# Kernel tuning notes

Measured on AMD Instinct MI355X. Metric: run time of the kernel, lower is better.

The kernel has to match this reference:

```python
import jax, jax.numpy as jnp
import numpy as np

T, K, E, H, I = 1024, 2, 8, 2048, 768


def setup_inputs() -> dict:
    key = jax.random.key(0)
    k1, k2, k3, k4, k5 = jax.random.split(key, 5)
    hidden_states = jax.random.normal(k1, (T, H), dtype=jnp.float32)
    top_k_index = jax.random.randint(k2, (T, K), 0, E)
    logits = jax.random.normal(k3, (T, K), dtype=jnp.float32)
    top_k_weights = jax.nn.softmax(logits, axis=-1)  # realistic routing weights
    # Linear-style weights: gate_up [E, 2I, H], down [E, H, I]; scaled like trained params
    gate_up_proj = jax.random.normal(k4, (E, 2 * I, H), dtype=jnp.float32) * 0.02
    down_proj = jax.random.normal(k5, (E, H, I), dtype=jnp.float32) * 0.02
    return {
        "hidden_states": hidden_states,
        "top_k_index": top_k_index,
        "top_k_weights": top_k_weights,
        "gate_up_proj": gate_up_proj,
        "down_proj": down_proj,
    }


def reference(hidden_states, top_k_index, top_k_weights, gate_up_proj, down_proj):
    """Dense-dispatch MoE forward: same math as the per-expert 4-bit loop.

    For every token t and routed expert e (with routing weight w):
      gate, up = split(x_t @ Wgu_e^T); y_t += w * (silu(gate)*up) @ Wd_e^T
    Expressed densely over experts; non-routed (token, expert) pairs get a
    combine weight of 0, so they contribute nothing.
    """
    num_experts = gate_up_proj.shape[0]
    # combine[t, e] = sum_k w[t,k] * [top_k_index[t,k] == e]
    combine = jnp.sum(
        jax.nn.one_hot(top_k_index, num_experts, dtype=hidden_states.dtype)
        * top_k_weights[..., None],
        axis=1,
    )  # [T, E]
    # gate_up: [T, E, 2I]
    gu = jnp.einsum("th,eoh->teo", hidden_states, gate_up_proj)
    gate, up = jnp.split(gu, 2, axis=-1)
    h = jax.nn.silu(gate) * up  # [T, E, I]
    # fold combine weight in before the down projection (scalar per (t,e))
    h = h * combine[:, :, None]
    out = jnp.einsum("tei,ehi->th", h, down_proj)  # [T, H]
    return out.astype(hidden_states.dtype)
```

## Files before the change

kernel.cpp:

```cpp
#include <hip/hip_runtime.h>
#include <hip/hip_bf16.h>

#define T_TOK 1024
#define TOPK  2
#define NEXP  8
#define HDIM  2048
#define IDIM  768
#define MROW  384

typedef __attribute__((ext_vector_type(4))) float f32x4;
typedef __attribute__((ext_vector_type(8))) short bf16x8;
typedef __attribute__((ext_vector_type(8))) unsigned short u16x8;
typedef __attribute__((ext_vector_type(8))) __bf16 bfv8;

__device__ __forceinline__ bf16x8 cvt8(f32x4 v0, f32x4 v1) {
  bfv8 r;
#pragma unroll
  for (int j = 0; j < 4; ++j) { r[j] = (__bf16)v0[j]; r[4 + j] = (__bf16)v1[j]; }
  return __builtin_bit_cast(bf16x8, r);
}

__device__ __forceinline__ void gload_lds16(const void* g, void* l) {
  __builtin_amdgcn_global_load_lds(
      (const __attribute__((address_space(1))) unsigned int*)((unsigned long long)g),
      (__attribute__((address_space(3))) unsigned int*)(unsigned int)(unsigned long long)(l),
      16, 0, 0);
}


__global__ void k_gather(const int* __restrict__ idx, const float* __restrict__ wts,
                         int* __restrict__ cnt, int* __restrict__ tok,
                         float* __restrict__ wl, int* __restrict__ inv) {
  int g = blockIdx.x * 256 + threadIdx.x;
  int e = idx[g];
  float w = wts[g];
  int pos = atomicAdd(&cnt[e], 1);
  if (pos < 2048) { tok[e * 2048 + pos] = g; wl[e * 2048 + pos] = w; }
  inv[g] = (pos < MROW) ? (e * MROW + pos) : -1;
}

__global__ __launch_bounds__(256) void k_compact(const float* __restrict__ x,
                                                 const int* __restrict__ inv,
                                                 unsigned short* __restrict__ xe) {
  int pid = blockIdx.x;
  int iv = inv[pid];
  if (iv < 0) return;
  const float* src = x + (size_t)(pid >> 1) * HDIM;
  unsigned short* dst = xe + (size_t)iv * HDIM;
  int i = threadIdx.x * 8;
  f32x4 a = *(const f32x4*)(src + i);
  f32x4 b = *(const f32x4*)(src + i + 4);
  *(u16x8*)(dst + i) = __builtin_bit_cast(u16x8, cvt8(a, b));
}

__global__ __launch_bounds__(256, 3) void k_gate_up(
    const unsigned short* __restrict__ xe, const float* __restrict__ Wgu,
    const int* __restrict__ cnt, const float* __restrict__ wl,
    unsigned short* __restrict__ hb)
{
  const int b = blockIdx.x;
  const int e = b & 7;
  const int r = b >> 3;
  const int mt = r % 6;
  const int nb = r / 6;
  const int m0 = mt * 64;
  int cc = cnt[e]; if (cc > MROW) cc = MROW;
  if (m0 >= cc) return;
  const int col0 = nb * 32;

  __shared__ unsigned short sA[3 * 4096];
  __shared__ unsigned short sB[3 * 4096];
  __shared__ float sW[64];

  const int tid = threadIdx.x;
  const int lane = tid & 63, wid = tid >> 6;

  if (tid < 64) sW[tid] = (m0 + tid < cc) ? wl[e * 2048 + m0 + tid] : 0.f;

  const unsigned short* xeE = xe + ((size_t)e * MROW + m0) * HDIM;
  const unsigned short* aSrc[2];
  unsigned int aDstOff[2];
#pragma unroll
  for (int i = 0; i < 2; ++i) {
    int row = wid * 16 + i * 8 + (lane >> 3);
    int csrc = (lane & 7) ^ (row & 7);
    aSrc[i] = xeE + (size_t)row * HDIM + csrc * 8;
    aDstOff[i] = (unsigned)(wid * 16 + i * 8) * 64;
  }

  const int brow = tid >> 2, cq = (tid & 3);
  const int ocol = (brow < 32) ? (col0 + brow) : (IDIM + col0 + (brow - 32));
  const float* bSrc = Wgu + ((size_t)e * 2 * IDIM + ocol) * HDIM + cq * 16;
  unsigned int bDst[2];
#pragma unroll
  for (int c2 = 0; c2 < 2; ++c2)
    bDst[c2] = (unsigned)(brow * 64 + (((cq * 2 + c2) ^ (brow & 7)) * 8));

  const int fl = lane & 15, q = lane >> 4;
  const int wm = (wid >> 1) * 32, wn = (wid & 1) * 16;

  f32x4 accg[2], accu[2];
#pragma unroll
  for (int mf = 0; mf < 2; ++mf) {
    accg[mf] = f32x4{0.f, 0.f, 0.f, 0.f};
    accu[mf] = f32x4{0.f, 0.f, 0.f, 0.f};
  }

  f32x4 blA[4], blB[4];
  const int NS = HDIM / 64;

  auto COMPUTE = [&](int bo) {
    const unsigned short* A = sA + bo;
    const unsigned short* B = sB + bo;
#pragma unroll
    for (int s = 0; s < 2; ++s) {
      bf16x8 a[2], g2, u2;
#pragma unroll
      for (int mf = 0; mf < 2; ++mf) {
        int rr = wm + mf * 16 + fl;
        a[mf] = *(const bf16x8*)(A + rr * 64 + (((s * 4 + q) ^ (rr & 7)) * 8));
      }
      {
        int rg = wn + fl;
        g2 = *(const bf16x8*)(B + rg * 64 + (((s * 4 + q) ^ (rg & 7)) * 8));
        int ru = 32 + wn + fl;
        u2 = *(const bf16x8*)(B + ru * 64 + (((s * 4 + q) ^ (ru & 7)) * 8));
      }
#pragma unroll
      for (int mf = 0; mf < 2; ++mf) {
        accg[mf] = __builtin_amdgcn_mfma_f32_16x16x32_bf16(a[mf], g2, accg[mf], 0, 0, 0);
        accu[mf] = __builtin_amdgcn_mfma_f32_16x16x32_bf16(a[mf], u2, accu[mf], 0, 0, 0);
      }
    }
  };

  auto ITER = [&](int ks, f32x4 (&blR)[4], f32x4 (&blW)[4],
                  int oC, int oN, int oNN) {
    const bool nL = (ks + 2) < NS;
    const bool nW = (ks + 1) < NS;
    if (nL) {
#pragma unroll
      for (int i = 0; i < 2; ++i)
        gload_lds16(aSrc[i] + (ks + 2) * 64, &sA[oNN + aDstOff[i]]);
#pragma unroll
      for (int j = 0; j < 4; ++j)
        blW[j] = *(const f32x4*)(bSrc + (ks + 2) * 64 + j * 4);
    }
    if (nW) {
#pragma unroll
      for (int c2 = 0; c2 < 2; ++c2)
        *(bf16x8*)&sB[oN + bDst[c2]] = cvt8(blR[c2 * 2], blR[c2 * 2 + 1]);
    }
    COMPUTE(oC);
    if (nW) {
      if (nL) { asm volatile("s_waitcnt vmcnt(6) lgkmcnt(0)" ::: "memory"); }
      else    { asm volatile("s_waitcnt vmcnt(0) lgkmcnt(0)" ::: "memory"); }
      __builtin_amdgcn_sched_barrier(0);
      __builtin_amdgcn_s_barrier();
      __builtin_amdgcn_sched_barrier(0);
    }
  };

#pragma unroll
  for (int i = 0; i < 2; ++i) gload_lds16(aSrc[i], &sA[aDstOff[i]]);
#pragma unroll
  for (int j = 0; j < 4; ++j) blA[j] = *(const f32x4*)(bSrc + j * 4);
#pragma unroll
  for (int i = 0; i < 2; ++i) gload_lds16(aSrc[i] + 64, &sA[4096 + aDstOff[i]]);
#pragma unroll
  for (int j = 0; j < 4; ++j) blB[j] = *(const f32x4*)(bSrc + 64 + j * 4);
#pragma unroll
  for (int c2 = 0; c2 < 2; ++c2)
    *(bf16x8*)&sB[bDst[c2]] = cvt8(blA[c2 * 2], blA[c2 * 2 + 1]);
  asm volatile("s_waitcnt vmcnt(6) lgkmcnt(0)" ::: "memory");
  __builtin_amdgcn_sched_barrier(0);
  __builtin_amdgcn_s_barrier();
  __builtin_amdgcn_sched_barrier(0);

  int oC = 0, oN = 4096, oNN = 8192;
  for (int ks = 0; ks < NS; ks += 2) {
    ITER(ks, blB, blA, oC, oN, oNN);
    int t = oC; oC = oN; oN = oNN; oNN = t;
    ITER(ks + 1, blA, blB, oC, oN, oNN);
    t = oC; oC = oN; oN = oNN; oNN = t;
  }

  unsigned short* hbE = hb + (size_t)e * MROW * IDIM;
  const int q4 = q * 4;
#pragma unroll
  for (int mf = 0; mf < 2; ++mf)
#pragma unroll
    for (int v = 0; v < 4; ++v) {
      int rowl = wm + mf * 16 + q4 + v;
      if (m0 + rowl < cc) {
        float g = accg[mf][v], u = accu[mf][v];
        float s = g / (1.f + __expf(-g));
        float h = s * u * sW[rowl];
        hbE[(size_t)(m0 + rowl) * IDIM + col0 + wn + fl] =
            __builtin_bit_cast(unsigned short, (__bf16)h);
      }
    }
}

__global__ __launch_bounds__(256, 3) void k_down(
    const unsigned short* __restrict__ hb, const float* __restrict__ Wd,
    const int* __restrict__ cnt, const int* __restrict__ tok,
    float* __restrict__ out)
{
  const int b = blockIdx.x;
  const int e = b & 7;
  const int r = b >> 3;
  const int mt = r % 6;
  const int nb = r / 6;
  const int m0 = mt * 64;
  int cc = cnt[e]; if (cc > MROW) cc = MROW;
  if (m0 >= cc) return;
  const int col0 = nb * 64;

  __shared__ unsigned short sA[3 * 4096];
  __shared__ unsigned short sB[3 * 4096];
  __shared__ int sTok[64];

  const int tid = threadIdx.x;
  const int lane = tid & 63, wid = tid >> 6;
  if (tid < 64) sTok[tid] = (m0 + tid < cc) ? (tok[e * 2048 + m0 + tid] >> 1) : 0;

  const unsigned short* hbE = hb + ((size_t)e * MROW + m0) * IDIM;
  const unsigned short* aSrc[2];
  unsigned int aDstOff[2];
#pragma unroll
  for (int i = 0; i < 2; ++i) {
    int row = wid * 16 + i * 8 + (lane >> 3);
    int csrc = (lane & 7) ^ (row & 7);
    aSrc[i] = hbE + (size_t)row * IDIM + csrc * 8;
    aDstOff[i] = (unsigned)(wid * 16 + i * 8) * 64;
  }

  const int brow = tid >> 2, cq = (tid & 3);
  const float* bSrc = Wd + ((size_t)e * HDIM + col0 + brow) * IDIM + cq * 16;
  unsigned int bDst[2];
#pragma unroll
  for (int c2 = 0; c2 < 2; ++c2)
    bDst[c2] = (unsigned)(brow * 64 + (((cq * 2 + c2) ^ (brow & 7)) * 8));

  const int fl = lane & 15, q = lane >> 4;
  const int wm = (wid >> 1) * 32, wn = (wid & 1) * 32;

  f32x4 acc[2][2];
#pragma unroll
  for (int mf = 0; mf < 2; ++mf)
#pragma unroll
    for (int nf = 0; nf < 2; ++nf) acc[mf][nf] = f32x4{0.f, 0.f, 0.f, 0.f};

  f32x4 blA[4], blB[4];
  const int NS = IDIM / 64;

  auto COMPUTE = [&](int bo) {
    const unsigned short* A = sA + bo;
    const unsigned short* B = sB + bo;
#pragma unroll
    for (int s = 0; s < 2; ++s) {
      bf16x8 a[2], bb[2];
#pragma unroll
      for (int mf = 0; mf < 2; ++mf) {
        int rr = wm + mf * 16 + fl;
        a[mf] = *(const bf16x8*)(A + rr * 64 + (((s * 4 + q) ^ (rr & 7)) * 8));
      }
#pragma unroll
      for (int nf = 0; nf < 2; ++nf) {
        int rn = wn + nf * 16 + fl;
        bb[nf] = *(const bf16x8*)(B + rn * 64 + (((s * 4 + q) ^ (rn & 7)) * 8));
      }
#pragma unroll
      for (int mf = 0; mf < 2; ++mf)
#pragma unroll
        for (int nf = 0; nf < 2; ++nf)
          acc[mf][nf] = __builtin_amdgcn_mfma_f32_16x16x32_bf16(a[mf], bb[nf], acc[mf][nf], 0, 0, 0);
    }
  };

  auto ITER = [&](int ks, f32x4 (&blR)[4], f32x4 (&blW)[4],
                  int oC, int oN, int oNN) {
    const bool nL = (ks + 2) < NS;
    const bool nW = (ks + 1) < NS;
    if (nL) {
#pragma unroll
      for (int i = 0; i < 2; ++i)
        gload_lds16(aSrc[i] + (ks + 2) * 64, &sA[oNN + aDstOff[i]]);
#pragma unroll
      for (int j = 0; j < 4; ++j)
        blW[j] = *(const f32x4*)(bSrc + (ks + 2) * 64 + j * 4);
    }
    if (nW) {
#pragma unroll
      for (int c2 = 0; c2 < 2; ++c2)
        *(bf16x8*)&sB[oN + bDst[c2]] = cvt8(blR[c2 * 2], blR[c2 * 2 + 1]);
    }
    COMPUTE(oC);
    if (nW) {
      if (nL) { asm volatile("s_waitcnt vmcnt(6) lgkmcnt(0)" ::: "memory"); }
      else    { asm volatile("s_waitcnt vmcnt(0) lgkmcnt(0)" ::: "memory"); }
      __builtin_amdgcn_sched_barrier(0);
      __builtin_amdgcn_s_barrier();
      __builtin_amdgcn_sched_barrier(0);
    }
  };

#pragma unroll
  for (int i = 0; i < 2; ++i) gload_lds16(aSrc[i], &sA[aDstOff[i]]);
#pragma unroll
  for (int j = 0; j < 4; ++j) blA[j] = *(const f32x4*)(bSrc + j * 4);
#pragma unroll
  for (int i = 0; i < 2; ++i) gload_lds16(aSrc[i] + 64, &sA[4096 + aDstOff[i]]);
#pragma unroll
  for (int j = 0; j < 4; ++j) blB[j] = *(const f32x4*)(bSrc + 64 + j * 4);
#pragma unroll
  for (int c2 = 0; c2 < 2; ++c2)
    *(bf16x8*)&sB[bDst[c2]] = cvt8(blA[c2 * 2], blA[c2 * 2 + 1]);
  asm volatile("s_waitcnt vmcnt(6) lgkmcnt(0)" ::: "memory");
  __builtin_amdgcn_sched_barrier(0);
  __builtin_amdgcn_s_barrier();
  __builtin_amdgcn_sched_barrier(0);

  int oC = 0, oN = 4096, oNN = 8192;
  for (int ks = 0; ks < NS; ks += 2) {
    ITER(ks, blB, blA, oC, oN, oNN);
    int t = oC; oC = oN; oN = oNN; oNN = t;
    ITER(ks + 1, blA, blB, oC, oN, oNN);
    t = oC; oC = oN; oN = oNN; oNN = t;
  }

  const int q4 = q * 4;
#pragma unroll
  for (int mf = 0; mf < 2; ++mf)
#pragma unroll
    for (int nf = 0; nf < 2; ++nf)
#pragma unroll
      for (int v = 0; v < 4; ++v) {
        int rowl = wm + mf * 16 + q4 + v;
        if (m0 + rowl < cc) {
          int t = sTok[rowl];
          atomicAdd(out + (size_t)t * HDIM + col0 + wn + nf * 16 + fl, acc[mf][nf][v]);
        }
      }
}

extern "C" void kernel_launch(void* const* d_in, const int* in_sizes, int n_in,
                              void* d_out, int out_size, void* d_ws, size_t ws_size,
                              hipStream_t stream) {
  const float* x   = (const float*)d_in[0];
  const int*   idx = (const int*)d_in[1];
  const float* wts = (const float*)d_in[2];
  const float* Wgu = (const float*)d_in[3];
  const float* Wd  = (const float*)d_in[4];
  float* out = (float*)d_out;

  char* ws = (char*)d_ws;
  int*            cnt = (int*)(ws + 0);
  int*            tok = (int*)(ws + 64);
  float*          wl  = (float*)(ws + 65600);
  int*            inv = (int*)(ws + 131136);
  unsigned short* xe  = (unsigned short*)(ws + 139328);
  unsigned short* hb  = (unsigned short*)(ws + 12722240);

  hipMemsetAsync(cnt, 0, NEXP * sizeof(int), stream);
  hipMemsetAsync(out, 0, (size_t)T_TOK * HDIM * sizeof(float), stream);
  k_gather<<<dim3((T_TOK * TOPK) / 256), 256, 0, stream>>>(idx, wts, cnt, tok, wl, inv);
  k_compact<<<dim3(T_TOK * TOPK), 256, 0, stream>>>(x, inv, xe);
  k_gate_up<<<dim3(NEXP * 6 * 24), 256, 0, stream>>>(xe, Wgu, cnt, wl, hb);
  k_down<<<dim3(NEXP * 6 * 32), 256, 0, stream>>>(hb, Wd, cnt, tok, out);
}
```

Baseline: 119.6 us.

## Enlarge gate_up M tile to 128 rows and simplify to double buffering

The gate_up kernel now covers 128 token rows per block instead of 64, so each fp32 weight tile loaded and converted is reused across twice as many rows, and the grid is halved. The triple-buffered pipeline with hand-placed waitcnt and barriers is replaced by a plain double-buffered loop synchronized with __syncthreads, and the occupancy hint in launch bounds is dropped. This cuts the redundant weight traffic, which dominates since weights are read in fp32, but gives up some load/compute overlap and leaves fewer blocks to fill the GPU.

New measurement: 108.7 us. 1.1x faster.

```diff
diff --git a/kernel.cpp b/kernel.cpp
--- a/kernel.cpp
+++ b/kernel.cpp
@@ -50,10 +50,10 @@
   int i = threadIdx.x * 8;
   f32x4 a = *(const f32x4*)(src + i);
   f32x4 b = *(const f32x4*)(src + i + 4);
-  *(u16x8*)(dst + i) = __builtin_bit_cast(u16x8, cvt8(a, b));
-}
-
-__global__ __launch_bounds__(256, 3) void k_gate_up(
+  *(bf16x8*)(dst + i) = cvt8(a, b);
+}
+
+__global__ __launch_bounds__(256) void k_gate_up(
     const unsigned short* __restrict__ xe, const float* __restrict__ Wgu,
     const int* __restrict__ cnt, const float* __restrict__ wl,
     unsigned short* __restrict__ hb)
@@ -61,31 +61,31 @@
   const int b = blockIdx.x;
   const int e = b & 7;
   const int r = b >> 3;
-  const int mt = r % 6;
-  const int nb = r / 6;
-  const int m0 = mt * 64;
+  const int mt = r % 3;
+  const int nb = r / 3;
+  const int m0 = mt * 128;
   int cc = cnt[e]; if (cc > MROW) cc = MROW;
   if (m0 >= cc) return;
   const int col0 = nb * 32;
 
-  __shared__ unsigned short sA[3 * 4096];
-  __shared__ unsigned short sB[3 * 4096];
-  __shared__ float sW[64];
+  __shared__ unsigned short sA[2][128 * 64];
+  __shared__ unsigned short sB[2][64 * 64];
+  __shared__ float sW[128];
 
   const int tid = threadIdx.x;
   const int lane = tid & 63, wid = tid >> 6;
 
-  if (tid < 64) sW[tid] = (m0 + tid < cc) ? wl[e * 2048 + m0 + tid] : 0.f;
+  if (tid < 128) sW[tid] = (m0 + tid < cc) ? wl[e * 2048 + m0 + tid] : 0.f;
 
   const unsigned short* xeE = xe + ((size_t)e * MROW + m0) * HDIM;
-  const unsigned short* aSrc[2];
-  unsigned int aDstOff[2];
-#pragma unroll
-  for (int i = 0; i < 2; ++i) {
-    int row = wid * 16 + i * 8 + (lane >> 3);
+  const unsigned short* aSrc[4];
+  unsigned int aDstOff[4];
+#pragma unroll
+  for (int i = 0; i < 4; ++i) {
+    int row = wid * 32 + i * 8 + (lane >> 3);
     int csrc = (lane & 7) ^ (row & 7);
     aSrc[i] = xeE + (size_t)row * HDIM + csrc * 8;
-    aDstOff[i] = (unsigned)(wid * 16 + i * 8) * 64;
+    aDstOff[i] = (unsigned)(wid * 32 + i * 8) * 64;
   }
 
   const int brow = tid >> 2, cq = (tid & 3);
@@ -97,28 +97,40 @@
     bDst[c2] = (unsigned)(brow * 64 + (((cq * 2 + c2) ^ (brow & 7)) * 8));
 
   const int fl = lane & 15, q = lane >> 4;
-  const int wm = (wid >> 1) * 32, wn = (wid & 1) * 16;
-
-  f32x4 accg[2], accu[2];
-#pragma unroll
-  for (int mf = 0; mf < 2; ++mf) {
-    accg[mf] = f32x4{0.f, 0.f, 0.f, 0.f};
-    accu[mf] = f32x4{0.f, 0.f, 0.f, 0.f};
-  }
-
-  f32x4 blA[4], blB[4];
-  const int NS = HDIM / 64;
-
-  auto COMPUTE = [&](int bo) {
-    const unsigned short* A = sA + bo;
-    const unsigned short* B = sB + bo;
+  const int wm = (wid >> 1) * 64, wn = (wid & 1) * 16;
+
+  f32x4 accg[4], accu[4];
+#pragma unroll
+  for (int rf = 0; rf < 4; ++rf) {
+    accg[rf] = f32x4{0.f, 0.f, 0.f, 0.f};
+    accu[rf] = f32x4{0.f, 0.f, 0.f, 0.f};
+  }
+
+  f32x4 bl[4];
+
+  auto STAGE_ISSUE = [&](int buf, int kt) {
+#pragma unroll
+    for (int i = 0; i < 4; ++i)
+      gload_lds16(aSrc[i] + kt, &sA[buf][aDstOff[i]]);
+#pragma unroll
+    for (int j = 0; j < 4; ++j)
+      bl[j] = *(const f32x4*)(bSrc + kt + j * 4);
+  };
+  auto STAGE_WRITE = [&](int buf) {
+#pragma unroll
+    for (int c2 = 0; c2 < 2; ++c2)
+      *(bf16x8*)&sB[buf][bDst[c2]] = cvt8(bl[c2 * 2], bl[c2 * 2 + 1]);
+  };
+  auto COMPUTE = [&](int buf) {
+    const unsigned short* A = sA[buf];
+    const unsigned short* B = sB[buf];
 #pragma unroll
     for (int s = 0; s < 2; ++s) {
-      bf16x8 a[2], g2, u2;
-#pragma unroll
-      for (int mf = 0; mf < 2; ++mf) {
-        int rr = wm + mf * 16 + fl;
-        a[mf] = *(const bf16x8*)(A + rr * 64 + (((s * 4 + q) ^ (rr & 7)) * 8));
+      bf16x8 a[4], g2, u2;
+#pragma unroll
+      for (int rf = 0; rf < 4; ++rf) {
+        int rr = wm + rf * 16 + fl;
+        a[rf] = *(const bf16x8*)(A + rr * 64 + (((s * 4 + q) ^ (rr & 7)) * 8));
       }
       {
         int rg = wn + fl;
@@ -127,73 +139,36 @@
         u2 = *(const bf16x8*)(B + ru * 64 + (((s * 4 + q) ^ (ru & 7)) * 8));
       }
 #pragma unroll
-      for (int mf = 0; mf < 2; ++mf) {
-        accg[mf] = __builtin_amdgcn_mfma_f32_16x16x32_bf16(a[mf], g2, accg[mf], 0, 0, 0);
-        accu[mf] = __builtin_amdgcn_mfma_f32_16x16x32_bf16(a[mf], u2, accu[mf], 0, 0, 0);
-      }
-    }
-  };
-
-  auto ITER = [&](int ks, f32x4 (&blR)[4], f32x4 (&blW)[4],
-                  int oC, int oN, int oNN) {
-    const bool nL = (ks + 2) < NS;
-    const bool nW = (ks + 1) < NS;
-    if (nL) {
-#pragma unroll
-      for (int i = 0; i < 2; ++i)
-        gload_lds16(aSrc[i] + (ks + 2) * 64, &sA[oNN + aDstOff[i]]);
-#pragma unroll
-      for (int j = 0; j < 4; ++j)
-        blW[j] = *(const f32x4*)(bSrc + (ks + 2) * 64 + j * 4);
-    }
-    if (nW) {
-#pragma unroll
-      for (int c2 = 0; c2 < 2; ++c2)
-        *(bf16x8*)&sB[oN + bDst[c2]] = cvt8(blR[c2 * 2], blR[c2 * 2 + 1]);
-    }
-    COMPUTE(oC);
-    if (nW) {
-      if (nL) { asm volatile("s_waitcnt vmcnt(6) lgkmcnt(0)" ::: "memory"); }
-      else    { asm volatile("s_waitcnt vmcnt(0) lgkmcnt(0)" ::: "memory"); }
-      __builtin_amdgcn_sched_barrier(0);
-      __builtin_amdgcn_s_barrier();
-      __builtin_amdgcn_sched_barrier(0);
-    }
-  };
-
-#pragma unroll
-  for (int i = 0; i < 2; ++i) gload_lds16(aSrc[i], &sA[aDstOff[i]]);
-#pragma unroll
-  for (int j = 0; j < 4; ++j) blA[j] = *(const f32x4*)(bSrc + j * 4);
-#pragma unroll
-  for (int i = 0; i < 2; ++i) gload_lds16(aSrc[i] + 64, &sA[4096 + aDstOff[i]]);
-#pragma unroll
-  for (int j = 0; j < 4; ++j) blB[j] = *(const f32x4*)(bSrc + 64 + j * 4);
-#pragma unroll
-  for (int c2 = 0; c2 < 2; ++c2)
-    *(bf16x8*)&sB[bDst[c2]] = cvt8(blA[c2 * 2], blA[c2 * 2 + 1]);
-  asm volatile("s_waitcnt vmcnt(6) lgkmcnt(0)" ::: "memory");
-  __builtin_amdgcn_sched_barrier(0);
-  __builtin_amdgcn_s_barrier();
-  __builtin_amdgcn_sched_barrier(0);
-
-  int oC = 0, oN = 4096, oNN = 8192;
-  for (int ks = 0; ks < NS; ks += 2) {
-    ITER(ks, blB, blA, oC, oN, oNN);
-    int t = oC; oC = oN; oN = oNN; oNN = t;
-    ITER(ks + 1, blA, blB, oC, oN, oNN);
-    t = oC; oC = oN; oN = oNN; oNN = t;
+      for (int rf = 0; rf < 4; ++rf) {
+        accg[rf] = __builtin_amdgcn_mfma_f32_16x16x32_bf16(a[rf], g2, accg[rf], 0, 0, 0);
+        accu[rf] = __builtin_amdgcn_mfma_f32_16x16x32_bf16(a[rf], u2, accu[rf], 0, 0, 0);
+      }
+    }
+  };
+
+  STAGE_ISSUE(0, 0);
+  STAGE_WRITE(0);
+  __syncthreads();
+  int buf = 0;
+  for (int kt = 0; kt < HDIM; kt += 64) {
+    const int nxt = kt + 64;
+    const bool more = nxt < HDIM;
+    if (more) STAGE_ISSUE(buf ^ 1, nxt);
+    COMPUTE(buf);
+    if (more) STAGE_WRITE(buf ^ 1);
+    __syncthreads();
+    buf ^= 1;
   }
 
   unsigned short* hbE = hb + (size_t)e * MROW * IDIM;
   const int q4 = q * 4;
 #pragma unroll
-  for (int mf = 0; mf < 2; ++mf)
+  for (int rf = 0; rf < 4; ++rf)
 #pragma unroll
     for (int v = 0; v < 4; ++v) {
-      int rowl = wm + mf * 16 + q4 + v;
+      int rowl = wm + rf * 16 + q4 + v;
       if (m0 + rowl < cc) {
-        float g = accg[mf][v], u = accu[mf][v];
+        float g = accg[rf][v], u = accu[rf][v];
         float s = g / (1.f + __expf(-g));
         float h = s * u * sW[rowl];
         hbE[(size_t)(m0 + rowl) * IDIM + col0 + wn + fl] =
@@ -367,6 +342,6 @@
   hipMemsetAsync(out, 0, (size_t)T_TOK * HDIM * sizeof(float), stream);
   k_gather<<<dim3((T_TOK * TOPK) / 256), 256, 0, stream>>>(idx, wts, cnt, tok, wl, inv);
   k_compact<<<dim3(T_TOK * TOPK), 256, 0, stream>>>(x, inv, xe);
-  k_gate_up<<<dim3(NEXP * 6 * 24), 256, 0, stream>>>(xe, Wgu, cnt, wl, hb);
+  k_gate_up<<<dim3(NEXP * 3 * 24), 256, 0, stream>>>(xe, Wgu, cnt, wl, hb);
   k_down<<<dim3(NEXP * 6 * 32), 256, 0, stream>>>(hb, Wd, cnt, tok, out);
 }
```
